# Performance work log

Hardware: AMD Instinct MI355X
Metric: run time of the kernel (lower is better)

Reference implementation:

```python
import jax, jax.numpy as jnp
import numpy as np

N = 100000
E = 1_600_000
DIN = 24
DH = 64
DOUT = 12
NEG_SLOPE = 0.01  # torch F.leaky_relu default


def setup_inputs() -> dict:
    key = jax.random.key(0)
    ks = jax.random.split(key, 18)
    inp = {}
    inp["feats"] = jax.random.normal(ks[0], (N, DIN), dtype=jnp.float32)
    inp["e_w"] = jax.random.uniform(ks[1], (E, 1), dtype=jnp.float32)
    inp["snorm_n"] = jnp.ones((N, 1), dtype=jnp.float32)
    inp["snorm_e"] = jnp.ones((E, 1), dtype=jnp.float32)
    inp["src"] = jax.random.randint(ks[2], (E,), 0, N, dtype=jnp.int32)
    inp["dst"] = jax.random.randint(ks[3], (E,), 0, N, dtype=jnp.int32)
    s = 0.05
    inp["emb_h_W"] = jax.random.normal(ks[4], (DH, DIN), dtype=jnp.float32) * s
    inp["emb_h_b"] = jnp.zeros((DH,), dtype=jnp.float32)
    inp["emb_e_W"] = jax.random.normal(ks[5], (DH, 1), dtype=jnp.float32) * s
    inp["emb_e_b"] = jnp.zeros((DH,), dtype=jnp.float32)
    inp["W_self1"] = jax.random.normal(ks[6], (DH, DH), dtype=jnp.float32) * s
    inp["W_func1"] = jax.random.normal(ks[7], (DH, DH), dtype=jnp.float32) * s
    inp["attn1"] = jax.random.normal(ks[8], (3 * DH,), dtype=jnp.float32) * s
    inp["W_self2"] = jax.random.normal(ks[9], (DH, DH), dtype=jnp.float32) * s
    inp["W_func2"] = jax.random.normal(ks[10], (DH, DH), dtype=jnp.float32) * s
    inp["attn2"] = jax.random.normal(ks[11], (3 * DH,), dtype=jnp.float32) * s
    inp["lin1_W"] = jax.random.normal(ks[12], (DOUT, DH), dtype=jnp.float32) * s
    inp["lin1_b"] = jnp.zeros((DOUT,), dtype=jnp.float32)
    return inp


def _gat_layer(h, w_edge, src, dst, W_self, W_func, attn):
    # h: [N, d], w_edge: [E, d] edge embedding, attn: [3d]
    h_s = h @ W_self.T                       # linear_self(h)
    z = h @ W_func.T                         # linear_func(h)
    d = z.shape[-1]
    a_src, a_dst, a_w = attn[:d], attn[d:2 * d], attn[2 * d:]
    # attention score: W_a . [z_src, z_dst, w]  (decomposed to avoid [E,3d] concat)
    s_node_src = z @ a_src                   # [N]
    s_node_dst = z @ a_dst                   # [N]
    e = s_node_src[src] + s_node_dst[dst] + w_edge @ a_w  # [E]
    e = jax.nn.leaky_relu(e, NEG_SLOPE)
    # segment softmax over incoming edges per destination node
    m = jax.ops.segment_max(e, dst, num_segments=h.shape[0])
    ex = jnp.exp(e - m[dst])
    denom = jax.ops.segment_sum(ex, dst, num_segments=h.shape[0])
    alpha = ex / denom[dst]                  # [E]
    msg = alpha[:, None] * z[src]            # [E, d]
    agg = jax.ops.segment_sum(msg, dst, num_segments=h.shape[0])  # [N, d]
    # DGL: nodes with no incoming edges keep their old 'h' (not h_s + agg)
    in_deg = jax.ops.segment_sum(jnp.ones_like(e), dst, num_segments=h.shape[0])
    h_mid = jnp.where((in_deg > 0)[:, None], h_s + agg, h)
    return h + jax.nn.relu(h_mid)            # relu then residual


def reference(feats, e_w, snorm_n, snorm_e, src, dst,
              emb_h_W, emb_h_b, emb_e_W, emb_e_b,
              W_self1, W_func1, attn1, W_self2, W_func2, attn2,
              lin1_W, lin1_b):
    feats = feats.reshape(feats.shape[0], -1)
    h = feats @ emb_h_W.T + emb_h_b          # [N, DH]
    e = e_w @ emb_e_W.T + emb_e_b            # [E, DH]
    h = _gat_layer(h, e, src, dst, W_self1, W_func1, attn1)
    h = _gat_layer(h, e, src, dst, W_self2, W_func2, attn2)
    y = h @ lin1_W.T + lin1_b                # [N, DOUT]
    return y
```

## Files before the change

### kernel.cpp

```cpp
#include <hip/hip_runtime.h>
#include <hip/hip_fp16.h>

#define N_NODES 100000
#define N_EDGES 1600000
#define DIN 24
#define DH 64
#define DOUT 12
#define NEG_SLOPE 0.01f
#define NG 32
#define EPG (N_EDGES / NG)
#define NS 7
#define SLICE_N 16384
#define NTOT (NG * N_NODES)
#define SCAN_BLK 4096
#define LDSW 72

#define NB_HIST (NS * NG)
#define NB_EMBED (((N_NODES * DH) + 8191) / 8192)
#define NB_SUMDEG ((N_NODES + 255) / 256)
#define NB_SCAN1N ((N_NODES + SCAN_BLK - 1) / SCAN_BLK)
#define NB_SCATTER (NG * 32)
#define BPE ((EPG + 31) / 32)
#define NB_NODE ((N_NODES + 63) / 64)
#define NB_AGG ((N_NODES + 7) / 8)

typedef _Float16 half8_t __attribute__((ext_vector_type(8)));
typedef float floatx4 __attribute__((ext_vector_type(4)));

__device__ __forceinline__ void dev_consts(const float* emb_e_W, const float* emb_e_b,
                                           const float* attn1, const float* attn2,
                                           float* consts) {
    int lane = threadIdx.x;
    if (lane >= 64) return;
    float w = emb_e_W[lane], b = emb_e_b[lane];
    float a1 = attn1[2 * DH + lane], a2 = attn2[2 * DH + lane];
    float c11 = w * a1, c01 = b * a1, c12 = w * a2, c02 = b * a2;
    for (int off = 32; off; off >>= 1) {
        c11 += __shfl_down(c11, off);
        c01 += __shfl_down(c01, off);
        c12 += __shfl_down(c12, off);
        c02 += __shfl_down(c02, off);
    }
    if (lane == 0) {
        consts[0] = c11; consts[1] = c01; consts[2] = c12; consts[3] = c02;
    }
}

__device__ __forceinline__ void dev_hist(int bid, const int* dst,
                                         unsigned char* deg, unsigned char* rank) {
    __shared__ unsigned cnt[SLICE_N / 4];
    int s = bid % NS, c = bid / NS;
    for (int i = threadIdx.x; i < SLICE_N / 4; i += 1024) cnt[i] = 0;
    __syncthreads();
    int nbase = s * SLICE_N;
    int start = c * EPG, end = start + EPG;
    for (int i = start + threadIdx.x; i < end; i += 1024) {
        int local = dst[i] - nbase;
        if ((unsigned)local < SLICE_N) {
            unsigned sh = (unsigned)(local & 3) * 8u;
            unsigned old = atomicAdd(&cnt[local >> 2], 1u << sh);
            rank[i] = (unsigned char)((old >> sh) & 255u);
        }
    }
    __syncthreads();
    int nmax = N_NODES - nbase;
    if (nmax > SLICE_N) nmax = SLICE_N;
    unsigned* dw = (unsigned*)(deg + (size_t)c * N_NODES + nbase);
    for (int l = threadIdx.x; l < (nmax >> 2); l += 1024) dw[l] = cnt[l];
}

__device__ __forceinline__ void dev_embed(int bid, const float* feats, const float* W,
                                          const float* b, float* h) {
    for (int r = 0; r < 8; ++r) {
        int idx = bid * 8192 + r * 1024 + threadIdx.x;
        if (idx >= N_NODES * DH) return;
        int n = idx >> 6, o = idx & 63;
        const float* f = feats + n * DIN;
        const float* w = W + o * DIN;
        float acc = b[o];
#pragma unroll
        for (int k = 0; k < DIN; ++k) acc += f[k] * w[k];
        h[idx] = acc;
    }
}

__device__ __forceinline__ void dev_scan1(int bid, const int* in, int* out,
                                          int* part, int n) {
    __shared__ int lds[256];
    int t = threadIdx.x;
    int base = bid * SCAN_BLK + t * 16;
    int v[16];
    int s = 0;
#pragma unroll
    for (int i = 0; i < 16; ++i) {
        int idx = base + i;
        v[i] = (idx < n) ? in[idx] : 0;
        s += v[i];
    }
    lds[t] = s;
    __syncthreads();
    for (int off = 1; off < 256; off <<= 1) {
        int y = (t >= off) ? lds[t - off] : 0;
        __syncthreads();
        lds[t] += y;
        __syncthreads();
    }
    int run = lds[t] - s;
#pragma unroll
    for (int i = 0; i < 16; ++i) {
        int idx = base + i;
        if (idx < n) out[idx] = run;
        run += v[i];
    }
    if (t == 255) part[bid] = lds[255];
}

__device__ __forceinline__ void dev_scan2(int* part, int nblk, int* row_offN) {
    __shared__ int lds2[256];
    int t = threadIdx.x;
    int v[4];
    int s = 0;
#pragma unroll
    for (int i = 0; i < 4; ++i) {
        int idx = t * 4 + i;
        v[i] = (idx < nblk) ? part[idx] : 0;
        s += v[i];
    }
    lds2[t] = s;
    __syncthreads();
    for (int off = 1; off < 256; off <<= 1) {
        int y = (t >= off) ? lds2[t - off] : 0;
        __syncthreads();
        lds2[t] += y;
        __syncthreads();
    }
    int run = lds2[t] - s;
#pragma unroll
    for (int i = 0; i < 4; ++i) {
        int idx = t * 4 + i;
        if (idx < nblk) part[idx] = run;
        run += v[i];
    }
    if (row_offN) {
        __syncthreads();
        if (t == 0) row_offN[N_NODES] = N_EDGES - part[N_NODES >> 12];
    }
}

__device__ __forceinline__ void dev_sumdeg(int bid, const unsigned char* degB,
                                           int* degN, unsigned char* chunkOff) {
    int n = bid * 256 + threadIdx.x;
    if (n >= N_NODES) return;
    int run = 0;
#pragma unroll
    for (int g = 0; g < NG; ++g) {
        size_t idx = (size_t)g * N_NODES + n;
        int v = (int)degB[idx];
        chunkOff[idx] = (unsigned char)run;
        run += v;
    }
    degN[n] = run;
}

__device__ __forceinline__ void dev_scatter(int bid, const int* src, const int* dst,
                                            const float* e_w, const unsigned char* rank,
                                            const int* row_offN, const int* partN,
                                            const unsigned char* chunkOff,
                                            unsigned* csr2) {
    int g = bid & 31, q = bid >> 5;
    int start = g * EPG + q * BPE;
    int end = start + BPE;
    int gend = (g + 1) * EPG;
    if (end > gend) end = gend;
    const unsigned char* co = chunkOff + (size_t)g * N_NODES;
    for (int i = start + threadIdx.x; i < end; i += 256) {
        int d = dst[i];
        unsigned qv = (unsigned)(e_w[i] * 32768.f);
        if (qv > 32767u) qv = 32767u;
        unsigned w = (unsigned)src[i] | (qv << 17);
        int pos = row_offN[d] + partN[d >> 12] + (int)co[d] + (int)rank[i];
        csr2[pos] = w;
    }
}

__device__ __forceinline__ void dev_node(int bid, const float* h,
                                         const float* Wself, const float* Wfunc,
                                         const float* attn,
                                         __half* zh, float* hs,
                                         float* s_src, float* s_dst) {
    __shared__ _Float16 lds[2 * 64 * LDSW];
    int tid = threadIdx.x;
    for (int idx = tid; idx < 2 * 64 * 64; idx += 256) {
        int mat = idx >> 12, rem = idx & 4095;
        int o = rem >> 6, k = rem & 63;
        float v = mat ? Wfunc[rem] : Wself[rem];
        lds[(mat * 64 + o) * LDSW + k] = (_Float16)v;
    }
    __syncthreads();

    int wave = tid >> 6, lane = tid & 63;
    int n0 = (bid * 4 + wave) * 16;
    if (n0 >= N_NODES) return;
    int quad = lane >> 4, lm = lane & 15;

    half8_t afrag[2];
    {
        const float4* hrow = (const float4*)(h + (size_t)(n0 + lm) * DH);
#pragma unroll
        for (int ks = 0; ks < 2; ++ks) {
            float4 p0 = hrow[ks * 8 + quad * 2];
            float4 p1 = hrow[ks * 8 + quad * 2 + 1];
            half8_t a;
            a[0] = (_Float16)p0.x; a[1] = (_Float16)p0.y;
            a[2] = (_Float16)p0.z; a[3] = (_Float16)p0.w;
            a[4] = (_Float16)p1.x; a[5] = (_Float16)p1.y;
            a[6] = (_Float16)p1.z; a[7] = (_Float16)p1.w;
            afrag[ks] = a;
        }
    }

    floatx4 accS[4], accF[4];
#pragma unroll
    for (int t = 0; t < 4; ++t) { accS[t] = (floatx4)0.f; accF[t] = (floatx4)0.f; }

    const _Float16* bS = lds;
    const _Float16* bF = lds + 64 * LDSW;
#pragma unroll
    for (int t = 0; t < 4; ++t) {
        int o = t * 16 + lm;
#pragma unroll
        for (int ks = 0; ks < 2; ++ks) {
            int hoff = o * LDSW + ks * 32 + quad * 8;
            half8_t b1 = *(const half8_t*)(bS + hoff);
            half8_t b2 = *(const half8_t*)(bF + hoff);
            accS[t] = __builtin_amdgcn_mfma_f32_16x16x32_f16(afrag[ks], b1, accS[t], 0, 0, 0);
            accF[t] = __builtin_amdgcn_mfma_f32_16x16x32_f16(afrag[ks], b2, accF[t], 0, 0, 0);
        }
    }

    float asv[4], adv[4];
#pragma unroll
    for (int t = 0; t < 4; ++t) {
        asv[t] = attn[t * 16 + lm];
        adv[t] = attn[DH + t * 16 + lm];
    }
    float ps[4] = {0.f, 0.f, 0.f, 0.f}, pd[4] = {0.f, 0.f, 0.f, 0.f};
#pragma unroll
    for (int t = 0; t < 4; ++t) {
#pragma unroll
        for (int r = 0; r < 4; ++r) {
            int node = n0 + quad * 4 + r;
            float zv = accF[t][r];
            zh[(size_t)node * DH + t * 16 + lm] = __float2half(zv);
            hs[(size_t)node * DH + t * 16 + lm] = accS[t][r];
            ps[r] += zv * asv[t];
            pd[r] += zv * adv[t];
        }
    }
#pragma unroll
    for (int r = 0; r < 4; ++r) {
        float p1 = ps[r], p2 = pd[r];
        for (int off = 8; off; off >>= 1) {
            p1 += __shfl_xor(p1, off);
            p2 += __shfl_xor(p2, off);
        }
        if (lm == 0) {
            s_src[n0 + quad * 4 + r] = p1;
            s_dst[n0 + quad * 4 + r] = p2;
        }
    }
}

__global__ void __launch_bounds__(1024, 2)
k_fuse1(const float* __restrict__ feats, const float* __restrict__ emb_h_W,
        const float* __restrict__ emb_h_b, float* __restrict__ h,
        const int* __restrict__ dst, unsigned char* __restrict__ deg,
        unsigned char* __restrict__ rank,
        const float* __restrict__ emb_e_W, const float* __restrict__ emb_e_b,
        const float* __restrict__ attn1, const float* __restrict__ attn2,
        float* __restrict__ consts) {
    int bid = blockIdx.x;
    if (bid == 0) { dev_consts(emb_e_W, emb_e_b, attn1, attn2, consts); return; }
    bid -= 1;
    if (bid < NB_HIST) { dev_hist(bid, dst, deg, rank); return; }
    dev_embed(bid - NB_HIST, feats, emb_h_W, emb_h_b, h);
}

__global__ void k_prep2(const unsigned char* __restrict__ degB, int* __restrict__ degN,
                        unsigned char* __restrict__ chunkOff) {
    dev_sumdeg(blockIdx.x, degB, degN, chunkOff);
}

__global__ void k_prep3(const int* __restrict__ degN, int* __restrict__ row_offN,
                        int* __restrict__ partN) {
    dev_scan1(blockIdx.x, degN, row_offN, partN, N_NODES);
}

__global__ void k_prep4(int* __restrict__ partN, int* __restrict__ row_offN) {
    dev_scan2(partN, NB_SCAN1N, row_offN);
}

__global__ void __launch_bounds__(256, 4)
k_fuse5(const int* __restrict__ src, const int* __restrict__ dst,
        const float* __restrict__ e_w, const unsigned char* __restrict__ rank,
        const int* __restrict__ row_offN, const int* __restrict__ partN,
        const unsigned char* __restrict__ chunkOff, unsigned* __restrict__ csr2,
        const float* __restrict__ h, const float* __restrict__ Wself1,
        const float* __restrict__ Wfunc1, const float* __restrict__ attn1,
        __half* __restrict__ zh, float* __restrict__ hs,
        float* __restrict__ s_src, float* __restrict__ s_dst) {
    int bid = blockIdx.x;
    if (bid < NB_SCATTER) {
        dev_scatter(bid, src, dst, e_w, rank, row_offN, partN, chunkOff, csr2);
        return;
    }
    dev_node(bid - NB_SCATTER, h, Wself1, Wfunc1, attn1, zh, hs, s_src, s_dst);
}

__global__ void __launch_bounds__(256, 4)
k_nodeL(const float* __restrict__ h, const float* __restrict__ Wself,
        const float* __restrict__ Wfunc, const float* __restrict__ attn,
        __half* __restrict__ zh, float* __restrict__ hs,
        float* __restrict__ s_src, float* __restrict__ s_dst) {
    dev_node(blockIdx.x, h, Wself, Wfunc, attn, zh, hs, s_src, s_dst);
}

__global__ void k_agg(const int* __restrict__ row_off, const int* __restrict__ partN,
                      const unsigned* __restrict__ csr,
                      const float* __restrict__ s_src, const float* __restrict__ s_dstA,
                      const float* __restrict__ consts, int layer,
                      const __half* __restrict__ zh, const float* __restrict__ hsb,
                      float* __restrict__ h,
                      const float* __restrict__ lin_W, const float* __restrict__ lin_b,
                      float* __restrict__ y, int final_layer) {
    int wave = threadIdx.x >> 6, lane = threadIdx.x & 63;
    int half = lane >> 5, hl = lane & 31;
    int eg = (lane >> 3) & 3, c8 = lane & 7;
    int n = blockIdx.x * 8 + wave * 2 + half;
    if (n >= N_NODES) return;
    int rs = row_off[n] + partN[n >> 12];
    int re = row_off[n + 1] + partN[(n + 1) >> 12];
    int deg = re - rs;
    int degO = __shfl_xor(deg, 32);
    int degmax = deg > degO ? deg : degO;

    float c1 = consts[layer * 2 + 0];
    float c0 = consts[layer * 2 + 1];
    float sd = s_dstA[n];

    float acc[8];
#pragma unroll
    for (int k = 0; k < 8; ++k) acc[k] = 0.f;
    float ssl = 0.f;
    int lbase = lane & 32;

    for (int base = 0; base < degmax; base += 32) {
        float ex = 0.f;
        int s0 = 0;
        int idx = base + hl;
        if (idx < deg) {
            unsigned w = csr[rs + idx];
            s0 = (int)(w & 0x1FFFFu);
            float ew = (float)(w >> 17) * (1.f / 32768.f);
            float e = s_src[s0] + sd + ew * c1 + c0;
            e = (e > 0.f) ? e : NEG_SLOPE * e;
            ex = __expf(e);
        }
        ssl += ex;
        int cnt = degmax - base;
        if (cnt > 32) cnt = 32;
#pragma unroll 4
        for (int jb = 0; jb < cnt; jb += 4) {
            int srcl = lbase + jb + eg;
            int sj = __shfl(s0, srcl);
            float exj = __shfl(ex, srcl);
            half8_t zv = *(const half8_t*)(zh + ((size_t)sj << 6) + (c8 << 3));
#pragma unroll
            for (int k = 0; k < 8; ++k) acc[k] += exj * (float)zv[k];
        }
    }
#pragma unroll
    for (int k = 0; k < 8; ++k) {
        acc[k] += __shfl_xor(acc[k], 8);
        acc[k] += __shfl_xor(acc[k], 16);
    }
    ssl += __shfl_xor(ssl, 16); ssl += __shfl_xor(ssl, 8);
    ssl += __shfl_xor(ssl, 4);  ssl += __shfl_xor(ssl, 2);
    ssl += __shfl_xor(ssl, 1);

    const float4* hp = (const float4*)(h + (size_t)n * DH);
    float4 ho0 = hp[c8 * 2], ho1 = hp[c8 * 2 + 1];
    float hold[8] = {ho0.x, ho0.y, ho0.z, ho0.w, ho1.x, ho1.y, ho1.z, ho1.w};
    float hnew[8];
    if (deg == 0) {
#pragma unroll
        for (int k = 0; k < 8; ++k) hnew[k] = hold[k] + fmaxf(hold[k], 0.f);
    } else {
        float rinv = 1.f / ssl;
        const float4* sp = (const float4*)(hsb + (size_t)n * DH);
        float4 hs0 = sp[c8 * 2], hs1 = sp[c8 * 2 + 1];
        float hsv[8] = {hs0.x, hs0.y, hs0.z, hs0.w, hs1.x, hs1.y, hs1.z, hs1.w};
#pragma unroll
        for (int k = 0; k < 8; ++k)
            hnew[k] = hold[k] + fmaxf(hsv[k] + acc[k] * rinv, 0.f);
    }

    if (!final_layer) {
        if (eg == 0) {
            float4* op = (float4*)(h + (size_t)n * DH);
            op[c8 * 2]     = make_float4(hnew[0], hnew[1], hnew[2], hnew[3]);
            op[c8 * 2 + 1] = make_float4(hnew[4], hnew[5], hnew[6], hnew[7]);
        }
    } else {
#pragma unroll
        for (int t = 0; t < 3; ++t) {
            int o = eg * 3 + t;
            const float* wr = lin_W + o * DH + c8 * 8;
            float p = 0.f;
#pragma unroll
            for (int k = 0; k < 8; ++k) p += hnew[k] * wr[k];
            p += __shfl_xor(p, 1); p += __shfl_xor(p, 2); p += __shfl_xor(p, 4);
            if (c8 == 0) y[n * DOUT + o] = p + lin_b[o];
        }
    }
}

extern "C" void kernel_launch(void* const* d_in, const int* in_sizes, int n_in,
                              void* d_out, int out_size, void* d_ws, size_t ws_size,
                              hipStream_t stream) {
    const float* feats   = (const float*)d_in[0];
    const float* e_w     = (const float*)d_in[1];
    const int*   src     = (const int*)d_in[4];
    const int*   dst     = (const int*)d_in[5];
    const float* emb_h_W = (const float*)d_in[6];
    const float* emb_h_b = (const float*)d_in[7];
    const float* emb_e_W = (const float*)d_in[8];
    const float* emb_e_b = (const float*)d_in[9];
    const float* Wself[2] = {(const float*)d_in[10], (const float*)d_in[13]};
    const float* Wfunc[2] = {(const float*)d_in[11], (const float*)d_in[14]};
    const float* attn[2]  = {(const float*)d_in[12], (const float*)d_in[15]};
    const float* lin1_W  = (const float*)d_in[16];
    const float* lin1_b  = (const float*)d_in[17];
    float* y = (float*)d_out;

    char* ws = (char*)d_ws;
    size_t off = 0;
    auto alloc = [&](size_t bytes) {
        void* p = ws + off;
        off += (bytes + 255) & ~(size_t)255;
        return p;
    };
    float*          h        = (float*)alloc((size_t)N_NODES * DH * 4);
    __half*         zh       = (__half*)alloc((size_t)N_NODES * DH * 2);
    float*          hs       = (float*)alloc((size_t)N_NODES * DH * 4);
    unsigned*       csr2     = (unsigned*)alloc((size_t)N_EDGES * 4);
    float*          s_src    = (float*)alloc((size_t)N_NODES * 4);
    float*          s_dst    = (float*)alloc((size_t)N_NODES * 4);
    int*            row_offN = (int*)alloc((size_t)(N_NODES + 1) * 4);
    unsigned char*  deg      = (unsigned char*)alloc((size_t)NTOT + 256);
    unsigned char*  chunkOff = (unsigned char*)alloc((size_t)NTOT + 256);
    unsigned char*  rank     = (unsigned char*)alloc((size_t)N_EDGES);
    int*            degN     = (int*)alloc((size_t)N_NODES * 4);
    int*            partN    = (int*)alloc(1024 * 4);
    float*          consts   = (float*)alloc(4 * 4);

    k_fuse1<<<1 + NB_HIST + NB_EMBED, 1024, 0, stream>>>(feats, emb_h_W, emb_h_b, h,
                                                         dst, deg, rank, emb_e_W, emb_e_b,
                                                         attn[0], attn[1], consts);
    k_prep2<<<NB_SUMDEG, 256, 0, stream>>>(deg, degN, chunkOff);
    k_prep3<<<NB_SCAN1N, 256, 0, stream>>>(degN, row_offN, partN);
    k_prep4<<<1, 256, 0, stream>>>(partN, row_offN);
    k_fuse5<<<NB_SCATTER + NB_NODE, 256, 0, stream>>>(
        src, dst, e_w, rank, row_offN, partN, chunkOff, csr2,
        h, Wself[0], Wfunc[0], attn[0], zh, hs, s_src, s_dst);
    k_agg<<<NB_AGG, 256, 0, stream>>>(row_offN, partN, csr2, s_src, s_dst, consts, 0,
                                      zh, hs, h, lin1_W, lin1_b, y, 0);
    k_nodeL<<<NB_NODE, 256, 0, stream>>>(h, Wself[1], Wfunc[1], attn[1],
                                         zh, hs, s_src, s_dst);
    k_agg<<<NB_AGG, 256, 0, stream>>>(row_offN, partN, csr2, s_src, s_dst, consts, 1,
                                      zh, hs, h, lin1_W, lin1_b, y, 1);
}
```

Measured before the change: 314.2 us.

## Merge two scan kernels via atomic flag spin-wait and raise occupancy bounds

The two-pass prefix scan over node degrees, previously two kernel launches, becomes one kernel. A final block spin-waits on an atomic counter, reset in the preceding kernel, until all partial-scan blocks have finished. This removes one launch and its gap. The change also raises the launch_bounds minimum-blocks hints for the node, fused scatter and aggregation kernels and adds unroll 2 to the scatter loop, which may force register limits or spills. The spin-wait relies on all scan blocks being co-resident or scheduled before the waiter, which holds for the small grid here.

```diff
diff --git a/kernel.cpp b/kernel.cpp
--- a/kernel.cpp
+++ b/kernel.cpp
@@ -173,6 +173,7 @@
     int gend = (g + 1) * EPG;
     if (end > gend) end = gend;
     const unsigned char* co = chunkOff + (size_t)g * N_NODES;
+#pragma unroll 2
     for (int i = start + threadIdx.x; i < end; i += 256) {
         int d = dst[i];
         unsigned qv = (unsigned)(e_w[i] * 32768.f);
@@ -287,20 +288,31 @@
 }
 
 __global__ void k_prep2(const unsigned char* __restrict__ degB, int* __restrict__ degN,
-                        unsigned char* __restrict__ chunkOff) {
+                        unsigned char* __restrict__ chunkOff, int* __restrict__ flag) {
+    if (blockIdx.x == 0 && threadIdx.x == 0) *flag = 0;
     dev_sumdeg(blockIdx.x, degB, degN, chunkOff);
 }
 
-__global__ void k_prep3(const int* __restrict__ degN, int* __restrict__ row_offN,
-                        int* __restrict__ partN) {
-    dev_scan1(blockIdx.x, degN, row_offN, partN, N_NODES);
-}
-
-__global__ void k_prep4(int* __restrict__ partN, int* __restrict__ row_offN) {
+__global__ void __launch_bounds__(256, 8)
+k_scan(const int* __restrict__ degN, int* __restrict__ row_offN,
+       int* __restrict__ partN, int* __restrict__ flag) {
+    int bid = blockIdx.x;
+    if (bid < NB_SCAN1N) {
+        dev_scan1(bid, degN, row_offN, partN, N_NODES);
+        __threadfence();
+        __syncthreads();
+        if (threadIdx.x == 0) atomicAdd(flag, 1);
+        return;
+    }
+    if (threadIdx.x == 0) {
+        while (atomicAdd(flag, 0) < NB_SCAN1N) __builtin_amdgcn_s_sleep(8);
+    }
+    __syncthreads();
+    __threadfence();
     dev_scan2(partN, NB_SCAN1N, row_offN);
 }
 
-__global__ void __launch_bounds__(256, 4)
+__global__ void __launch_bounds__(256, 6)
 k_fuse5(const int* __restrict__ src, const int* __restrict__ dst,
         const float* __restrict__ e_w, const unsigned char* __restrict__ rank,
         const int* __restrict__ row_offN, const int* __restrict__ partN,
@@ -317,7 +329,7 @@
     dev_node(bid - NB_SCATTER, h, Wself1, Wfunc1, attn1, zh, hs, s_src, s_dst);
 }
 
-__global__ void __launch_bounds__(256, 4)
+__global__ void __launch_bounds__(256, 6)
 k_nodeL(const float* __restrict__ h, const float* __restrict__ Wself,
         const float* __restrict__ Wfunc, const float* __restrict__ attn,
         __half* __restrict__ zh, float* __restrict__ hs,
@@ -325,14 +337,15 @@
     dev_node(blockIdx.x, h, Wself, Wfunc, attn, zh, hs, s_src, s_dst);
 }
 
-__global__ void k_agg(const int* __restrict__ row_off, const int* __restrict__ partN,
-                      const unsigned* __restrict__ csr,
-                      const float* __restrict__ s_src, const float* __restrict__ s_dstA,
-                      const float* __restrict__ consts, int layer,
-                      const __half* __restrict__ zh, const float* __restrict__ hsb,
-                      float* __restrict__ h,
-                      const float* __restrict__ lin_W, const float* __restrict__ lin_b,
-                      float* __restrict__ y, int final_layer) {
+__global__ void __launch_bounds__(256, 8)
+k_agg(const int* __restrict__ row_off, const int* __restrict__ partN,
+      const unsigned* __restrict__ csr,
+      const float* __restrict__ s_src, const float* __restrict__ s_dstA,
+      const float* __restrict__ consts, int layer,
+      const __half* __restrict__ zh, const float* __restrict__ hsb,
+      float* __restrict__ h,
+      const float* __restrict__ lin_W, const float* __restrict__ lin_b,
+      float* __restrict__ y, int final_layer) {
     int wave = threadIdx.x >> 6, lane = threadIdx.x & 63;
     int half = lane >> 5, hl = lane & 31;
     int eg = (lane >> 3) & 3, c8 = lane & 7;
@@ -463,13 +476,13 @@
     int*            degN     = (int*)alloc((size_t)N_NODES * 4);
     int*            partN    = (int*)alloc(1024 * 4);
     float*          consts   = (float*)alloc(4 * 4);
+    int*            flag     = (int*)alloc(4 * 4);
 
     k_fuse1<<<1 + NB_HIST + NB_EMBED, 1024, 0, stream>>>(feats, emb_h_W, emb_h_b, h,
                                                          dst, deg, rank, emb_e_W, emb_e_b,
                                                          attn[0], attn[1], consts);
-    k_prep2<<<NB_SUMDEG, 256, 0, stream>>>(deg, degN, chunkOff);
-    k_prep3<<<NB_SCAN1N, 256, 0, stream>>>(degN, row_offN, partN);
-    k_prep4<<<1, 256, 0, stream>>>(partN, row_offN);
+    k_prep2<<<NB_SUMDEG, 256, 0, stream>>>(deg, degN, chunkOff, flag);
+    k_scan<<<NB_SCAN1N + 1, 256, 0, stream>>>(degN, row_offN, partN, flag);
     k_fuse5<<<NB_SCATTER + NB_NODE, 256, 0, stream>>>(
         src, dst, e_w, rank, row_offN, partN, chunkOff, csr2,
         h, Wself[0], Wfunc[0], attn[0], zh, hs, s_src, s_dst);
```

After: 333.7 us. 1.06x slower.

## Move layer-1 node transform into degree-sum kernel and split edge scatter out

Applied to the files above, without the earlier changes.

The first-layer node transform (MFMA linear + attention scores) now runs alongside the per-node degree summation instead of alongside the CSR scatter. The scatter becomes its own flat one-thread-per-edge kernel. The node transform loops over two tiles per block, which halves the block count and the number of weight-to-LDS conversions. The aim is to overlap compute with the small prep kernel and to give the scatter full-device parallelism, at the cost of one more launch plus index division in the scatter.

```diff
diff --git a/kernel.cpp b/kernel.cpp
--- a/kernel.cpp
+++ b/kernel.cpp
@@ -19,9 +19,9 @@
 #define NB_EMBED (((N_NODES * DH) + 8191) / 8192)
 #define NB_SUMDEG ((N_NODES + 255) / 256)
 #define NB_SCAN1N ((N_NODES + SCAN_BLK - 1) / SCAN_BLK)
-#define NB_SCATTER (NG * 32)
-#define BPE ((EPG + 31) / 32)
+#define NB_SCAT ((N_EDGES + 255) / 256)
 #define NB_NODE ((N_NODES + 63) / 64)
+#define NB_NODE_T ((NB_NODE + 1) / 2)
 #define NB_AGG ((N_NODES + 7) / 8)
 
 typedef _Float16 half8_t __attribute__((ext_vector_type(8)));
@@ -162,32 +162,11 @@
     degN[n] = run;
 }
 
-__device__ __forceinline__ void dev_scatter(int bid, const int* src, const int* dst,
-                                            const float* e_w, const unsigned char* rank,
-                                            const int* row_offN, const int* partN,
-                                            const unsigned char* chunkOff,
-                                            unsigned* csr2) {
-    int g = bid & 31, q = bid >> 5;
-    int start = g * EPG + q * BPE;
-    int end = start + BPE;
-    int gend = (g + 1) * EPG;
-    if (end > gend) end = gend;
-    const unsigned char* co = chunkOff + (size_t)g * N_NODES;
-    for (int i = start + threadIdx.x; i < end; i += 256) {
-        int d = dst[i];
-        unsigned qv = (unsigned)(e_w[i] * 32768.f);
-        if (qv > 32767u) qv = 32767u;
-        unsigned w = (unsigned)src[i] | (qv << 17);
-        int pos = row_offN[d] + partN[d >> 12] + (int)co[d] + (int)rank[i];
-        csr2[pos] = w;
-    }
-}
-
-__device__ __forceinline__ void dev_node(int bid, const float* h,
-                                         const float* Wself, const float* Wfunc,
-                                         const float* attn,
-                                         __half* zh, float* hs,
-                                         float* s_src, float* s_dst) {
+__device__ __forceinline__ void dev_nodeM(int bid, int stride, const float* h,
+                                          const float* Wself, const float* Wfunc,
+                                          const float* attn,
+                                          __half* zh, float* hs,
+                                          float* s_src, float* s_dst) {
     __shared__ _Float16 lds[2 * 64 * LDSW];
     int tid = threadIdx.x;
     for (int idx = tid; idx < 2 * 64 * 64; idx += 256) {
@@ -199,74 +178,77 @@
     __syncthreads();
 
     int wave = tid >> 6, lane = tid & 63;
-    int n0 = (bid * 4 + wave) * 16;
-    if (n0 >= N_NODES) return;
     int quad = lane >> 4, lm = lane & 15;
-
-    half8_t afrag[2];
-    {
-        const float4* hrow = (const float4*)(h + (size_t)(n0 + lm) * DH);
-#pragma unroll
-        for (int ks = 0; ks < 2; ++ks) {
-            float4 p0 = hrow[ks * 8 + quad * 2];
-            float4 p1 = hrow[ks * 8 + quad * 2 + 1];
-            half8_t a;
-            a[0] = (_Float16)p0.x; a[1] = (_Float16)p0.y;
-            a[2] = (_Float16)p0.z; a[3] = (_Float16)p0.w;
-            a[4] = (_Float16)p1.x; a[5] = (_Float16)p1.y;
-            a[6] = (_Float16)p1.z; a[7] = (_Float16)p1.w;
-            afrag[ks] = a;
-        }
-    }
-
-    floatx4 accS[4], accF[4];
-#pragma unroll
-    for (int t = 0; t < 4; ++t) { accS[t] = (floatx4)0.f; accF[t] = (floatx4)0.f; }
-
-    const _Float16* bS = lds;
-    const _Float16* bF = lds + 64 * LDSW;
-#pragma unroll
-    for (int t = 0; t < 4; ++t) {
-        int o = t * 16 + lm;
-#pragma unroll
-        for (int ks = 0; ks < 2; ++ks) {
-            int hoff = o * LDSW + ks * 32 + quad * 8;
-            half8_t b1 = *(const half8_t*)(bS + hoff);
-            half8_t b2 = *(const half8_t*)(bF + hoff);
-            accS[t] = __builtin_amdgcn_mfma_f32_16x16x32_f16(afrag[ks], b1, accS[t], 0, 0, 0);
-            accF[t] = __builtin_amdgcn_mfma_f32_16x16x32_f16(afrag[ks], b2, accF[t], 0, 0, 0);
-        }
-    }
-
     float asv[4], adv[4];
 #pragma unroll
     for (int t = 0; t < 4; ++t) {
         asv[t] = attn[t * 16 + lm];
         adv[t] = attn[DH + t * 16 + lm];
     }
-    float ps[4] = {0.f, 0.f, 0.f, 0.f}, pd[4] = {0.f, 0.f, 0.f, 0.f};
-#pragma unroll
-    for (int t = 0; t < 4; ++t) {
+    const _Float16* bS = lds;
+    const _Float16* bF = lds + 64 * LDSW;
+
+    for (int tb = bid; tb < NB_NODE; tb += stride) {
+        int n0 = (tb * 4 + wave) * 16;
+        if (n0 >= N_NODES) continue;
+
+        half8_t afrag[2];
+        {
+            const float4* hrow = (const float4*)(h + (size_t)(n0 + lm) * DH);
+#pragma unroll
+            for (int ks = 0; ks < 2; ++ks) {
+                float4 p0 = hrow[ks * 8 + quad * 2];
+                float4 p1 = hrow[ks * 8 + quad * 2 + 1];
+                half8_t a;
+                a[0] = (_Float16)p0.x; a[1] = (_Float16)p0.y;
+                a[2] = (_Float16)p0.z; a[3] = (_Float16)p0.w;
+                a[4] = (_Float16)p1.x; a[5] = (_Float16)p1.y;
+                a[6] = (_Float16)p1.z; a[7] = (_Float16)p1.w;
+                afrag[ks] = a;
+            }
+        }
+
+        floatx4 accS[4], accF[4];
+#pragma unroll
+        for (int t = 0; t < 4; ++t) { accS[t] = (floatx4)0.f; accF[t] = (floatx4)0.f; }
+
+#pragma unroll
+        for (int t = 0; t < 4; ++t) {
+            int o = t * 16 + lm;
+#pragma unroll
+            for (int ks = 0; ks < 2; ++ks) {
+                int hoff = o * LDSW + ks * 32 + quad * 8;
+                half8_t b1 = *(const half8_t*)(bS + hoff);
+                half8_t b2 = *(const half8_t*)(bF + hoff);
+                accS[t] = __builtin_amdgcn_mfma_f32_16x16x32_f16(afrag[ks], b1, accS[t], 0, 0, 0);
+                accF[t] = __builtin_amdgcn_mfma_f32_16x16x32_f16(afrag[ks], b2, accF[t], 0, 0, 0);
+            }
+        }
+
+        float ps[4] = {0.f, 0.f, 0.f, 0.f}, pd[4] = {0.f, 0.f, 0.f, 0.f};
+#pragma unroll
+        for (int t = 0; t < 4; ++t) {
+#pragma unroll
+            for (int r = 0; r < 4; ++r) {
+                int node = n0 + quad * 4 + r;
+                float zv = accF[t][r];
+                zh[(size_t)node * DH + t * 16 + lm] = __float2half(zv);
+                hs[(size_t)node * DH + t * 16 + lm] = accS[t][r];
+                ps[r] += zv * asv[t];
+                pd[r] += zv * adv[t];
+            }
+        }
 #pragma unroll
         for (int r = 0; r < 4; ++r) {
-            int node = n0 + quad * 4 + r;
-            float zv = accF[t][r];
-            zh[(size_t)node * DH + t * 16 + lm] = __float2half(zv);
-            hs[(size_t)node * DH + t * 16 + lm] = accS[t][r];
-            ps[r] += zv * asv[t];
-            pd[r] += zv * adv[t];
-        }
-    }
-#pragma unroll
-    for (int r = 0; r < 4; ++r) {
-        float p1 = ps[r], p2 = pd[r];
-        for (int off = 8; off; off >>= 1) {
-            p1 += __shfl_xor(p1, off);
-            p2 += __shfl_xor(p2, off);
-        }
-        if (lm == 0) {
-            s_src[n0 + quad * 4 + r] = p1;
-            s_dst[n0 + quad * 4 + r] = p2;
+            float p1 = ps[r], p2 = pd[r];
+            for (int off = 8; off; off >>= 1) {
+                p1 += __shfl_xor(p1, off);
+                p2 += __shfl_xor(p2, off);
+            }
+            if (lm == 0) {
+                s_src[n0 + quad * 4 + r] = p1;
+                s_dst[n0 + quad * 4 + r] = p2;
+            }
         }
     }
 }
@@ -286,35 +268,43 @@
     dev_embed(bid - NB_HIST, feats, emb_h_W, emb_h_b, h);
 }
 
-__global__ void k_prep2(const unsigned char* __restrict__ degB, int* __restrict__ degN,
-                        unsigned char* __restrict__ chunkOff) {
-    dev_sumdeg(blockIdx.x, degB, degN, chunkOff);
-}
-
-__global__ void k_prep3(const int* __restrict__ degN, int* __restrict__ row_offN,
-                        int* __restrict__ partN) {
-    dev_scan1(blockIdx.x, degN, row_offN, partN, N_NODES);
-}
-
-__global__ void k_prep4(int* __restrict__ partN, int* __restrict__ row_offN) {
-    dev_scan2(partN, NB_SCAN1N, row_offN);
-}
-
 __global__ void __launch_bounds__(256, 4)
-k_fuse5(const int* __restrict__ src, const int* __restrict__ dst,
-        const float* __restrict__ e_w, const unsigned char* __restrict__ rank,
-        const int* __restrict__ row_offN, const int* __restrict__ partN,
-        const unsigned char* __restrict__ chunkOff, unsigned* __restrict__ csr2,
+k_fuse2(const unsigned char* __restrict__ degB, int* __restrict__ degN,
+        unsigned char* __restrict__ chunkOff,
         const float* __restrict__ h, const float* __restrict__ Wself1,
         const float* __restrict__ Wfunc1, const float* __restrict__ attn1,
         __half* __restrict__ zh, float* __restrict__ hs,
         float* __restrict__ s_src, float* __restrict__ s_dst) {
     int bid = blockIdx.x;
-    if (bid < NB_SCATTER) {
-        dev_scatter(bid, src, dst, e_w, rank, row_offN, partN, chunkOff, csr2);
-        return;
-    }
-    dev_node(bid - NB_SCATTER, h, Wself1, Wfunc1, attn1, zh, hs, s_src, s_dst);
+    if (bid < NB_SUMDEG) { dev_sumdeg(bid, degB, degN, chunkOff); return; }
+    dev_nodeM(bid - NB_SUMDEG, NB_NODE_T, h, Wself1, Wfunc1, attn1,
+              zh, hs, s_src, s_dst);
+}
+
+__global__ void k_prep3(const int* __restrict__ degN, int* __restrict__ row_offN,
+                        int* __restrict__ partN) {
+    dev_scan1(blockIdx.x, degN, row_offN, partN, N_NODES);
+}
+
+__global__ void k_prep4(int* __restrict__ partN, int* __restrict__ row_offN) {
+    dev_scan2(partN, NB_SCAN1N, row_offN);
+}
+
+__global__ void __launch_bounds__(256, 8)
+k_scat(const int* __restrict__ src, const int* __restrict__ dst,
+       const float* __restrict__ e_w, const unsigned char* __restrict__ rank,
+       const int* __restrict__ row_offN, const int* __restrict__ partN,
+       const unsigned char* __restrict__ chunkOff, unsigned* __restrict__ csr2) {
+    int i = blockIdx.x * 256 + threadIdx.x;
+    if (i >= N_EDGES) return;
+    int g = i / EPG;
+    int d = dst[i];
+    unsigned qv = (unsigned)(e_w[i] * 32768.f);
+    if (qv > 32767u) qv = 32767u;
+    unsigned w = (unsigned)src[i] | (qv << 17);
+    int pos = row_offN[d] + partN[d >> 12] + (int)chunkOff[(size_t)g * N_NODES + d]
+            + (int)rank[i];
+    csr2[pos] = w;
 }
 
 __global__ void __launch_bounds__(256, 4)
@@ -322,7 +312,7 @@
         const float* __restrict__ Wfunc, const float* __restrict__ attn,
         __half* __restrict__ zh, float* __restrict__ hs,
         float* __restrict__ s_src, float* __restrict__ s_dst) {
-    dev_node(blockIdx.x, h, Wself, Wfunc, attn, zh, hs, s_src, s_dst);
+    dev_nodeM(blockIdx.x, NB_NODE_T, h, Wself, Wfunc, attn, zh, hs, s_src, s_dst);
 }
 
 __global__ void k_agg(const int* __restrict__ row_off, const int* __restrict__ partN,
@@ -467,16 +457,16 @@
     k_fuse1<<<1 + NB_HIST + NB_EMBED, 1024, 0, stream>>>(feats, emb_h_W, emb_h_b, h,
                                                          dst, deg, rank, emb_e_W, emb_e_b,
                                                          attn[0], attn[1], consts);
-    k_prep2<<<NB_SUMDEG, 256, 0, stream>>>(deg, degN, chunkOff);
+    k_fuse2<<<NB_SUMDEG + NB_NODE_T, 256, 0, stream>>>(
+        deg, degN, chunkOff, h, Wself[0], Wfunc[0], attn[0], zh, hs, s_src, s_dst);
     k_prep3<<<NB_SCAN1N, 256, 0, stream>>>(degN, row_offN, partN);
     k_prep4<<<1, 256, 0, stream>>>(partN, row_offN);
-    k_fuse5<<<NB_SCATTER + NB_NODE, 256, 0, stream>>>(
-        src, dst, e_w, rank, row_offN, partN, chunkOff, csr2,
-        h, Wself[0], Wfunc[0], attn[0], zh, hs, s_src, s_dst);
+    k_scat<<<NB_SCAT, 256, 0, stream>>>(src, dst, e_w, rank, row_offN, partN,
+                                        chunkOff, csr2);
     k_agg<<<NB_AGG, 256, 0, stream>>>(row_offN, partN, csr2, s_src, s_dst, consts, 0,
                                       zh, hs, h, lin1_W, lin1_b, y, 0);
-    k_nodeL<<<NB_NODE, 256, 0, stream>>>(h, Wself[1], Wfunc[1], attn[1],
-                                         zh, hs, s_src, s_dst);
+    k_nodeL<<<NB_NODE_T, 256, 0, stream>>>(h, Wself[1], Wfunc[1], attn[1],
+                                           zh, hs, s_src, s_dst);
     k_agg<<<NB_AGG, 256, 0, stream>>>(row_offN, partN, csr2, s_src, s_dst, consts, 1,
                                       zh, hs, h, lin1_W, lin1_b, y, 1);
 }
```

Result: slower. 339.3 us (+8.0%).
